# Kernel tuning notes

Hardware: AMD Instinct MI355X
Metric: run time of the kernel (lower is better)

The kernel has to match this reference:

```python
import jax, jax.numpy as jnp
import numpy as np

DATA_DIM = 768
HIDDEN = 768
STEPS = 100
DEPTH = 4          # eqx MLP depth=4 -> 4 hidden layers (3 width->width linears)
STATE = 4 * DATA_DIM
RTOL, ATOL = 1e-3, 1e-6
SAFETY, FMIN, FMAX, DT0 = 0.9, 0.2, 10.0, 0.1
INNER = 6          # bounded adaptive attempts per save interval (differentiable)

# Tsit5 Butcher tableau
A21 = 0.161
A31, A32 = -0.008480655492356989, 0.335480655492357
A41, A42, A43 = 2.8971530571054935, -6.359448489975075, 4.3622954328695815
A51, A52, A53, A54 = 5.325864828439257, -11.748883564062828, 7.4955393428898365, -0.09249506636175525
A61, A62, A63, A64, A65 = 5.86145544294642, -12.92096931784711, 8.159367898576159, -0.071584973281401, -0.028269050394068383
B1, B2, B3, B4, B5, B6 = 0.09646076681806523, 0.01, 0.4798896504144996, 1.379008574103742, -3.290069515436081, 2.324710524099774
E1, E2, E3, E4, E5, E6, E7 = -0.001780011052226, -0.000816434459657, 0.007880878010262, -0.144711007173263, 0.582357165452555, -0.458082105929187, 0.015151515151515152


def _mlp(y, W_in, b_in, W_hid, b_hid, W_out, b_out):
    h = jax.nn.softplus(W_in @ y + b_in)
    for i in range(W_hid.shape[0]):
        h = jax.nn.softplus(W_hid[i] @ h + b_hid[i])
    return W_out @ h + b_out


def _tsit5_step(f, y, dt):
    k1 = f(y)
    k2 = f(y + dt * (A21 * k1))
    k3 = f(y + dt * (A31 * k1 + A32 * k2))
    k4 = f(y + dt * (A41 * k1 + A42 * k2 + A43 * k3))
    k5 = f(y + dt * (A51 * k1 + A52 * k2 + A53 * k3 + A54 * k4))
    k6 = f(y + dt * (A61 * k1 + A62 * k2 + A63 * k3 + A64 * k4 + A65 * k5))
    y1 = y + dt * (B1 * k1 + B2 * k2 + B3 * k3 + B4 * k4 + B5 * k5 + B6 * k6)
    k7 = f(y1)
    e = dt * (E1 * k1 + E2 * k2 + E3 * k3 + E4 * k4 + E5 * k5 + E6 * k6 + E7 * k7)
    scale = ATOL + RTOL * jnp.maximum(jnp.abs(y), jnp.abs(y1))
    err = jnp.sqrt(jnp.mean((e / scale) ** 2))
    return y1, err


def _integrate(f, y0, ts):
    # adaptive Tsit5 with I-controller; step exactly to each save time
    def interval(carry, t1):
        def attempt(c, _):
            t, y, dt = c
            done = t >= t1 - 1e-10
            dt_eff = jnp.where(done, dt, jnp.minimum(dt, t1 - t))
            y1, err = _tsit5_step(f, y, dt_eff)
            accept = (err <= 1.0) & (~done)
            t_n = jnp.where(accept, t + dt_eff, t)
            y_n = jnp.where(accept, y1, y)
            factor = jnp.clip(SAFETY * jnp.maximum(err, 1e-10) ** (-0.2), FMIN, FMAX)
            dt_n = jnp.where(done, dt, dt_eff * factor)
            return (t_n, y_n, dt_n), None
        (t, y, dt), _ = jax.lax.scan(attempt, carry, None, length=INNER)
        return (t1, y, dt), y
    carry0 = (ts[0], y0, jnp.asarray(DT0, y0.dtype))
    _, ys = jax.lax.scan(interval, carry0, ts[1:])
    return jnp.concatenate([y0[None], ys], axis=0)  # [steps, STATE]


def setup_inputs() -> dict:
    key = jax.random.key(0)
    ks = jax.random.split(key, 12)

    def lin(kw, kb, fan_in, fan_out):  # equinox Linear init: U(-1/sqrt(in), 1/sqrt(in))
        lim = 1.0 / float(np.sqrt(fan_in))
        W = jax.random.uniform(kw, (fan_out, fan_in), minval=-lim, maxval=lim, dtype=jnp.float32)
        b = jax.random.uniform(kb, (fan_out,), minval=-lim, maxval=lim, dtype=jnp.float32)
        return W, b

    W_in, b_in = lin(ks[0], ks[1], STATE, HIDDEN)
    Wh, bh = [], []
    for i in range(DEPTH - 1):
        W, b = lin(ks[2 + 2 * i], ks[3 + 2 * i], HIDDEN, HIDDEN)
        Wh.append(W)
        bh.append(b)
    W_hid, b_hid = jnp.stack(Wh), jnp.stack(bh)
    W_out, b_out = lin(ks[8], ks[9], HIDDEN, STATE)
    y0 = jax.random.normal(ks[10], (STATE,), dtype=jnp.float32) * 0.01
    eps = jax.random.normal(ks[11], (STEPS, DATA_DIM), dtype=jnp.float32)
    return {"y0": y0, "W_in": W_in, "b_in": b_in, "W_hid": W_hid, "b_hid": b_hid,
            "W_out": W_out, "b_out": b_out, "eps": eps, "steps": STEPS}


def reference(y0, W_in, b_in, W_hid, b_hid, W_out, b_out, eps, steps):
    ts = jnp.linspace(0.0, 1.0, steps)
    f = lambda y: _mlp(y, W_in, b_in, W_hid, b_hid, W_out, b_out)
    ys = _integrate(f, y0, ts)                 # [steps, 4*data_dim]
    means = ys[:, :DATA_DIM]
    stddevs = ys[:, DATA_DIM:2 * DATA_DIM]
    return means + eps * stddevs               # [steps, data_dim]
```

## Files before the change

### kernel.cpp

```cpp
#include <hip/hip_runtime.h>
#include <math.h>

#define NBLK 96
#define BLK  512
#define NSTATE 3072
#define HID  768
typedef unsigned long long u64;
typedef unsigned int u32;

__device__ const float d_AT[7][6] = {
  {0.f,0.f,0.f,0.f,0.f,0.f},
  {0.161f,0.f,0.f,0.f,0.f,0.f},
  {-0.008480655492356989f,0.335480655492357f,0.f,0.f,0.f,0.f},
  {2.8971530571054935f,-6.359448489975075f,4.3622954328695815f,0.f,0.f,0.f},
  {5.325864828439257f,-11.748883564062828f,7.4955393428898365f,-0.09249506636175525f,0.f,0.f},
  {5.86145544294642f,-12.92096931784711f,8.159367898576159f,-0.071584973281401f,-0.028269050394068383f,0.f},
  {0.09646076681806523f,0.01f,0.4798896504144996f,1.379008574103742f,-3.290069515436081f,2.324710524099774f},
};
__device__ const float d_EC[7] = {
  -0.001780011052226f,-0.000816434459657f,0.007880878010262f,-0.144711007173263f,
   0.582357165452555f,-0.458082105929187f,0.015151515151515152f };

namespace {
constexpr float SBc = 0.09646076681806523f+0.01f+0.4798896504144996f
                    +1.379008574103742f+(-3.290069515436081f)+2.324710524099774f;
constexpr float SEc = -0.001780011052226f-0.000816434459657f+0.007880878010262f
                      -0.144711007173263f+0.582357165452555f-0.458082105929187f
                      +0.015151515151515152f;
}

struct GT { u64 h[2][HID]; u64 p[2][NBLK]; };
__device__ GT gt;
__device__ int g_abort;
__device__ __align__(16) float g_M[HID*HID];
__device__ float g_c0[HID];

__global__ void reset_kernel(){
  u64* w = reinterpret_cast<u64*>(&gt);
  const int n = (int)(sizeof(GT)/8);
  for (int i = blockIdx.x*blockDim.x + threadIdx.x; i < n; i += gridDim.x*blockDim.x)
    __hip_atomic_store(w + i, 0ull, __ATOMIC_RELAXED, __HIP_MEMORY_SCOPE_AGENT);
  if (blockIdx.x == 0 && threadIdx.x == 0)
    __hip_atomic_store(&g_abort, 0, __ATOMIC_RELAXED, __HIP_MEMORY_SCOPE_AGENT);
}

__global__ __launch_bounds__(512)
void prep_kernel(const float* __restrict__ Win, const float* __restrict__ Wout,
                 const float* __restrict__ bout){
  const int blk = blockIdx.x;
  const int t = threadIdx.x;
  const int rl = t >> 6, lane = t & 63;
  const int r = blk*8 + rl;
  {
    const float4* wr = reinterpret_cast<const float4*>(Win + (size_t)r*NSTATE) + lane;
    const float4* bo = reinterpret_cast<const float4*>(bout) + lane;
    float acc = 0.f;
    #pragma unroll
    for (int i = 0; i < 12; ++i){
      float4 w = wr[64*i], b = bo[64*i];
      acc = fmaf(w.x,b.x, fmaf(w.y,b.y, fmaf(w.z,b.z, fmaf(w.w,b.w, acc))));
    }
    acc += __shfl_xor(acc,32); acc += __shfl_xor(acc,16); acc += __shfl_xor(acc,8);
    acc += __shfl_xor(acc,4);  acc += __shfl_xor(acc,2);  acc += __shfl_xor(acc,1);
    if (lane == 0) g_c0[r] = acc;
  }
  const int cb = (t & 63) * 12;
  float acc[12];
  #pragma unroll
  for (int m = 0; m < 12; ++m) acc[m] = 0.f;
  const float* wrow = Win + (size_t)r*NSTATE;
  for (int i = 0; i < NSTATE; ++i){
    const float wv = wrow[i];
    const float4* wo = reinterpret_cast<const float4*>(Wout + (size_t)i*HID + cb);
    float4 a0 = wo[0], a1 = wo[1], a2 = wo[2];
    acc[0]=fmaf(wv,a0.x,acc[0]); acc[1]=fmaf(wv,a0.y,acc[1]);
    acc[2]=fmaf(wv,a0.z,acc[2]); acc[3]=fmaf(wv,a0.w,acc[3]);
    acc[4]=fmaf(wv,a1.x,acc[4]); acc[5]=fmaf(wv,a1.y,acc[5]);
    acc[6]=fmaf(wv,a1.z,acc[6]); acc[7]=fmaf(wv,a1.w,acc[7]);
    acc[8]=fmaf(wv,a2.x,acc[8]); acc[9]=fmaf(wv,a2.y,acc[9]);
    acc[10]=fmaf(wv,a2.z,acc[10]); acc[11]=fmaf(wv,a2.w,acc[11]);
  }
  #pragma unroll
  for (int m = 0; m < 12; ++m) g_M[(size_t)r*HID + cb + m] = acc[m];
}

__device__ __forceinline__ int abort_now(){
  return __hip_atomic_load(&g_abort, __ATOMIC_RELAXED, __HIP_MEMORY_SCOPE_AGENT);
}
__device__ __forceinline__ void raise_abort(){
  __hip_atomic_store(&g_abort, 1, __ATOMIC_RELAXED, __HIP_MEMORY_SCOPE_AGENT);
}
__device__ __forceinline__ void stT(u64* p, u32 tag, float v){
  u32 b; __builtin_memcpy(&b, &v, 4);
  __hip_atomic_store(p, ((u64)tag << 32) | (u64)b, __ATOMIC_RELAXED, __HIP_MEMORY_SCOPE_AGENT);
}
__device__ __forceinline__ float pollT1(const u64* p, u32 tag){
  u64* q = const_cast<u64*>(p);
  u64 w = __hip_atomic_load(q, __ATOMIC_RELAXED, __HIP_MEMORY_SCOPE_AGENT);
  u32 guard = 0;
  while ((u32)(w >> 32) != tag){
    if ((guard & 63u) == 63u && abort_now()) break;
    if (++guard > (1u<<16)){ raise_abort(); break; }
    __builtin_amdgcn_s_sleep(1);
    w = __hip_atomic_load(q, __ATOMIC_RELAXED, __HIP_MEMORY_SCOPE_AGENT);
  }
  u32 b = (u32)w; float v; __builtin_memcpy(&v, &b, 4); return v;
}
template<int NW, int CNT>
__device__ __forceinline__ void pollW(const u64* src, u32 tag, float* dst){
  const int tid = threadIdx.x;
  u64* s = const_cast<u64*>(src);
  u64 w[NW];
  #pragma unroll
  for (int r = 0; r < NW; ++r){
    const int i = tid + BLK*r;
    w[r] = (i < CNT) ? __hip_atomic_load(s + i, __ATOMIC_RELAXED, __HIP_MEMORY_SCOPE_AGENT)
                     : ((u64)tag << 32);
  }
  u32 guard = 0;
  for (;;){
    bool all = true;
    #pragma unroll
    for (int r = 0; r < NW; ++r) if ((u32)(w[r] >> 32) != tag) all = false;
    if (all) break;
    if ((guard & 63u) == 63u && abort_now()) break;
    if (++guard > (1u<<16)){ raise_abort(); break; }
    __builtin_amdgcn_s_sleep(1);
    #pragma unroll
    for (int r = 0; r < NW; ++r){
      const int i = tid + BLK*r;
      if (i < CNT && (u32)(w[r] >> 32) != tag)
        w[r] = __hip_atomic_load(s + i, __ATOMIC_RELAXED, __HIP_MEMORY_SCOPE_AGENT);
    }
  }
  #pragma unroll
  for (int r = 0; r < NW; ++r){
    const int i = tid + BLK*r;
    if (i < CNT){ u32 b = (u32)w[r]; float v; __builtin_memcpy(&v, &b, 4); dst[i] = v; }
  }
}

__device__ __forceinline__ float softplus_f(float x){
  return fmaxf(x, 0.0f) + log1pf(expf(-fabsf(x)));
}

__global__ __launch_bounds__(BLK)
void ode_kernel(const float* __restrict__ y0p,
                const float* __restrict__ Win,  const float* __restrict__ bin,
                const float* __restrict__ Whid, const float* __restrict__ bhid,
                const float* __restrict__ Wout, const float* __restrict__ bout,
                const float* __restrict__ eps,  float* __restrict__ out)
{
  __shared__ float h4s[8][HID];
  __shared__ float hsh[HID];
  __shared__ float hBs[HID], hEs[HID];
  __shared__ float us[8][8];
  __shared__ float vsl[8], b1s[8];
  __shared__ float ysl[32], y1sl[32], esl[32];
  __shared__ float red[8];
  __shared__ int s_ab;

  const int tid  = threadIdx.x, blk = blockIdx.x;
  const int wave = tid >> 6, lane = tid & 63;
  const int l16  = lane & 15;
  const int ro   = tid >> 4;
  const int row1 = blk*8 + wave;
  const int orow = (ro >> 3)*HID + blk*8 + (ro & 7);
  const int gi   = (tid >> 3)*HID + blk*8 + (tid & 7);

  float4 wr0[3], wr1[3], wr2[3], mreg[3];
  {
    const float4* b0 = reinterpret_cast<const float4*>(Whid + ((size_t)0*HID + row1)*HID) + lane;
    const float4* b1 = reinterpret_cast<const float4*>(Whid + ((size_t)1*HID + row1)*HID) + lane;
    const float4* b2 = reinterpret_cast<const float4*>(Whid + ((size_t)2*HID + row1)*HID) + lane;
    const float4* mb = reinterpret_cast<const float4*>(g_M  + (size_t)row1*HID) + lane;
    #pragma unroll
    for (int i = 0; i < 3; ++i){
      wr0[i] = b0[64*i]; wr1[i] = b1[64*i]; wr2[i] = b2[64*i]; mreg[i] = mb[64*i];
    }
  }
  const float4* wo  = reinterpret_cast<const float4*>(Wout + (size_t)orow*HID) + l16;
  const float bh0 = bhid[row1], bh1 = bhid[HID+row1], bh2 = bhid[2*HID+row1];
  const float c0r = g_c0[row1];
  const float bo_r = bout[orow];

  if (tid < 32) ysl[tid] = y0p[gi];
  if (lane == 0) b1s[wave] = bin[row1];
  if (tid < 8){ const int e = blk*8 + tid; out[e] = y0p[e] + eps[e]*y0p[HID+e]; }
  {
    float* scratch = &h4s[0][0];
    float4* d4 = reinterpret_cast<float4*>(scratch);
    const float4* s4 = reinterpret_cast<const float4*>(y0p);
    #pragma unroll
    for (int r = 0; r < 2; ++r){ const int i = tid + BLK*r; if (i < NSTATE/4) d4[i] = s4[i]; }
    __syncthreads();
    const float4* wr = reinterpret_cast<const float4*>(Win + (size_t)row1*NSTATE) + lane;
    const float4* zl = reinterpret_cast<const float4*>(scratch) + lane;
    float acc = 0.f;
    #pragma unroll
    for (int i = 0; i < 12; ++i){
      float4 w = wr[64*i], x = zl[64*i];
      acc = fmaf(w.x,x.x, fmaf(w.y,x.y, fmaf(w.z,x.z, fmaf(w.w,x.w, acc))));
    }
    acc += __shfl_xor(acc,32); acc += __shfl_xor(acc,16); acc += __shfl_xor(acc,8);
    acc += __shfl_xor(acc,4);  acc += __shfl_xor(acc,2);  acc += __shfl_xor(acc,1);
    if (lane == 0) vsl[wave] = acc;
    __syncthreads();
  }

  u32 hseq = 0, pseq = 0;
  int kpar = 0;
  auto slot = [&](int j){ return (j==1) ? (kpar?7:1) : (j==7) ? (kpar?1:7) : j; };

  auto stage = [&](int s, float dte){
    __syncthreads();
    const int tg = slot(s + 1);
    ++hseq;
    if (tid < 8){
      float a = 0.f;
      for (int j = 1; j <= s; ++j) a += d_AT[s][j-1] * us[slot(j)][tid];
      stT(&gt.h[hseq&1][blk*8 + tid], hseq, softplus_f(vsl[tid] + dte*a + b1s[tid]));
    }
    pollW<2, HID>(gt.h[hseq&1], hseq, hsh);
    __syncthreads();
    #pragma unroll
    for (int l = 0; l < 3; ++l){
      const float4* hx = reinterpret_cast<const float4*>(hsh) + lane;
      float acc = 0.f;
      #pragma unroll
      for (int i = 0; i < 3; ++i){
        float4 w = (l==0) ? wr0[i] : (l==1) ? wr1[i] : wr2[i];
        float4 x = hx[64*i];
        acc = fmaf(w.x,x.x, fmaf(w.y,x.y, fmaf(w.z,x.z, fmaf(w.w,x.w, acc))));
      }
      acc += __shfl_xor(acc,32); acc += __shfl_xor(acc,16); acc += __shfl_xor(acc,8);
      acc += __shfl_xor(acc,4);  acc += __shfl_xor(acc,2);  acc += __shfl_xor(acc,1);
      const float bh = (l==0) ? bh0 : (l==1) ? bh1 : bh2;
      ++hseq;
      if (lane == 0) stT(&gt.h[hseq&1][row1], hseq, softplus_f(acc + bh));
      __syncthreads();
      pollW<2, HID>(gt.h[hseq&1], hseq, (l < 2) ? hsh : h4s[tg]);
      __syncthreads();
    }
    {
      const float4* hx = reinterpret_cast<const float4*>(h4s[tg]) + lane;
      float acc = 0.f;
      #pragma unroll
      for (int i = 0; i < 3; ++i){
        float4 w = mreg[i], x = hx[64*i];
        acc = fmaf(w.x,x.x, fmaf(w.y,x.y, fmaf(w.z,x.z, fmaf(w.w,x.w, acc))));
      }
      acc += __shfl_xor(acc,32); acc += __shfl_xor(acc,16); acc += __shfl_xor(acc,8);
      acc += __shfl_xor(acc,4);  acc += __shfl_xor(acc,2);  acc += __shfl_xor(acc,1);
      if (lane == 0) us[tg][wave] = acc + c0r;
    }
  };

  stage(0, 0.f);

  float t = 0.f, dtv = 0.1f;
  for (int iv = 1; iv < 100; ++iv){
    const float t1 = (float)iv / 99.0f;
    for (int a = 0; a < 6; ++a){
      if (t >= t1 - 1e-10f) break;
      if (tid == 0) s_ab = abort_now();
      __syncthreads();
      if (s_ab) return;
      const float dte = fminf(dtv, t1 - t);

      stage(1,dte); stage(2,dte); stage(3,dte);
      stage(4,dte); stage(5,dte); stage(6,dte);
      __syncthreads();

      for (int c = tid; c < HID; c += BLK){
        float hb = 0.f, he = 0.f;
        for (int j = 1; j <= 6; ++j) hb = fmaf(d_AT[6][j-1], h4s[slot(j)][c], hb);
        for (int j = 1; j <= 7; ++j) he = fmaf(d_EC[j-1],    h4s[slot(j)][c], he);
        hBs[c] = hb; hEs[c] = he;
      }
      __syncthreads();
      {
        const float4* hb4 = reinterpret_cast<const float4*>(hBs) + l16;
        const float4* he4 = reinterpret_cast<const float4*>(hEs) + l16;
        float ab = 0.f, ae = 0.f;
        #pragma unroll
        for (int i = 0; i < 12; ++i){
          float4 w = wo[16*i], xb = hb4[16*i], xe = he4[16*i];
          ab = fmaf(w.x,xb.x, fmaf(w.y,xb.y, fmaf(w.z,xb.z, fmaf(w.w,xb.w, ab))));
          ae = fmaf(w.x,xe.x, fmaf(w.y,xe.y, fmaf(w.z,xe.z, fmaf(w.w,xe.w, ae))));
        }
        ab += __shfl_xor(ab,8); ab += __shfl_xor(ab,4); ab += __shfl_xor(ab,2); ab += __shfl_xor(ab,1);
        ae += __shfl_xor(ae,8); ae += __shfl_xor(ae,4); ae += __shfl_xor(ae,2); ae += __shfl_xor(ae,1);
        if (l16 == 0){
          y1sl[ro] = ysl[ro] + dte*(ab + SBc*bo_r);
          esl[ro]  = dte*(ae + SEc*bo_r);
        }
      }
      __syncthreads();
      ++pseq;
      if (tid < 32){
        const float sc = 1e-6f + 1e-3f * fmaxf(fabsf(ysl[tid]), fabsf(y1sl[tid]));
        const float q = esl[tid] / sc;
        float v = q*q;
        v += __shfl_xor(v,16); v += __shfl_xor(v,8);
        v += __shfl_xor(v,4);  v += __shfl_xor(v,2); v += __shfl_xor(v,1);
        if (tid == 0) stT(&gt.p[pseq&1][blk], pseq, v);
      }
      float v = 0.f;
      if (tid < NBLK) v = pollT1(&gt.p[pseq&1][tid], pseq);
      v += __shfl_xor(v,32); v += __shfl_xor(v,16); v += __shfl_xor(v,8);
      v += __shfl_xor(v,4);  v += __shfl_xor(v,2);  v += __shfl_xor(v,1);
      if (lane == 0) red[wave] = v;
      __syncthreads();
      const float err = sqrtf((red[0]+red[1]) * (1.0f/3072.0f));
      __syncthreads();

      const bool accept = (err <= 1.0f);
      const float factor = fminf(fmaxf(0.9f * powf(fmaxf(err, 1e-10f), -0.2f), 0.2f), 10.0f);
      if (accept){
        t += dte;
        if (tid < 32) ysl[tid] = y1sl[tid];
        if (tid < 8){
          float s = 0.f;
          for (int j = 1; j <= 6; ++j) s += d_AT[6][j-1] * us[slot(j)][tid];
          vsl[tid] += dte * s;
        }
        kpar ^= 1;
      }
      dtv = dte * factor;
      __syncthreads();
    }
    t = t1;
    if (tid < 8){
      const int m = blk*8 + tid;
      out[(size_t)iv*HID + m] = ysl[tid] + eps[(size_t)iv*HID + m] * ysl[8 + tid];
    }
    __syncthreads();
  }
}

extern "C" void kernel_launch(void* const* d_in, const int* in_sizes, int n_in,
                              void* d_out, int out_size, void* d_ws, size_t ws_size,
                              hipStream_t stream) {
  const float* y0   = (const float*)d_in[0];
  const float* Win  = (const float*)d_in[1];
  const float* bin  = (const float*)d_in[2];
  const float* Whid = (const float*)d_in[3];
  const float* bhid = (const float*)d_in[4];
  const float* Wout = (const float*)d_in[5];
  const float* bout = (const float*)d_in[6];
  const float* eps  = (const float*)d_in[7];
  float* out = (float*)d_out;
  (void)in_sizes; (void)n_in; (void)out_size; (void)d_ws; (void)ws_size;

  reset_kernel<<<dim3(4), dim3(BLK), 0, stream>>>();
  prep_kernel<<<dim3(96), dim3(512), 0, stream>>>(Win, Wout, bout);
  ode_kernel<<<dim3(NBLK), dim3(BLK), 0, stream>>>(y0, Win, bin, Whid, bhid, Wout, bout, eps, out);
}
```

Baseline: 7.839 ms.

## Halve persistent grid to 48 blocks and retile precompute GEMM with LDS-staged Win

```diff
diff --git a/kernel.cpp b/kernel.cpp
--- a/kernel.cpp
+++ b/kernel.cpp
@@ -1,7 +1,7 @@
 #include <hip/hip_runtime.h>
 #include <math.h>
 
-#define NBLK 96
+#define NBLK 48
 #define BLK  512
 #define NSTATE 3072
 #define HID  768
@@ -44,44 +44,68 @@
     __hip_atomic_store(&g_abort, 0, __ATOMIC_RELAXED, __HIP_MEMORY_SCOPE_AGENT);
 }
 
-__global__ __launch_bounds__(512)
+__global__ __launch_bounds__(512, 1)
 void prep_kernel(const float* __restrict__ Win, const float* __restrict__ Wout,
                  const float* __restrict__ bout){
+  extern __shared__ float wl[];
   const int blk = blockIdx.x;
   const int t = threadIdx.x;
-  const int rl = t >> 6, lane = t & 63;
-  const int r = blk*8 + rl;
   {
+    const float4* wsrc = reinterpret_cast<const float4*>(Win + (size_t)blk*8*NSTATE);
+    float4* wdst = reinterpret_cast<float4*>(wl);
+    for (int i = t; i < 8*NSTATE/4; i += 512) wdst[i] = wsrc[i];
+  }
+  __syncthreads();
+  const int seg = t >> 6;
+  const int cb  = (t & 63) * 12;
+  float acc[8][12];
+  #pragma unroll
+  for (int r = 0; r < 8; ++r)
+    #pragma unroll
+    for (int j = 0; j < 12; ++j) acc[r][j] = 0.f;
+  const int k0 = seg * 384;
+  for (int k = 0; k < 384; ++k){
+    const float4* wo4 = reinterpret_cast<const float4*>(Wout + (size_t)(k0 + k)*HID + cb);
+    const float4 a0 = wo4[0], a1 = wo4[1], a2 = wo4[2];
+    #pragma unroll
+    for (int r = 0; r < 8; ++r){
+      const float wv = wl[r*NSTATE + k0 + k];
+      acc[r][0]=fmaf(wv,a0.x,acc[r][0]); acc[r][1]=fmaf(wv,a0.y,acc[r][1]);
+      acc[r][2]=fmaf(wv,a0.z,acc[r][2]); acc[r][3]=fmaf(wv,a0.w,acc[r][3]);
+      acc[r][4]=fmaf(wv,a1.x,acc[r][4]); acc[r][5]=fmaf(wv,a1.y,acc[r][5]);
+      acc[r][6]=fmaf(wv,a1.z,acc[r][6]); acc[r][7]=fmaf(wv,a1.w,acc[r][7]);
+      acc[r][8]=fmaf(wv,a2.x,acc[r][8]); acc[r][9]=fmaf(wv,a2.y,acc[r][9]);
+      acc[r][10]=fmaf(wv,a2.z,acc[r][10]); acc[r][11]=fmaf(wv,a2.w,acc[r][11]);
+    }
+  }
+  __syncthreads();
+  for (int r = 0; r < 8; ++r){
+    #pragma unroll
+    for (int j = 0; j < 12; ++j) wl[seg*HID + cb + j] = acc[r][j];
+    __syncthreads();
+    for (int c = t; c < HID; c += 512){
+      float s2 = 0.f;
+      #pragma unroll
+      for (int s3 = 0; s3 < 8; ++s3) s2 += wl[s3*HID + c];
+      g_M[(size_t)(blk*8 + r)*HID + c] = s2;
+    }
+    __syncthreads();
+  }
+  {
+    const int rl = t >> 6, lane = t & 63;
+    const int r = blk*8 + rl;
     const float4* wr = reinterpret_cast<const float4*>(Win + (size_t)r*NSTATE) + lane;
     const float4* bo = reinterpret_cast<const float4*>(bout) + lane;
-    float acc = 0.f;
+    float a2c = 0.f;
     #pragma unroll
     for (int i = 0; i < 12; ++i){
       float4 w = wr[64*i], b = bo[64*i];
-      acc = fmaf(w.x,b.x, fmaf(w.y,b.y, fmaf(w.z,b.z, fmaf(w.w,b.w, acc))));
-    }
-    acc += __shfl_xor(acc,32); acc += __shfl_xor(acc,16); acc += __shfl_xor(acc,8);
-    acc += __shfl_xor(acc,4);  acc += __shfl_xor(acc,2);  acc += __shfl_xor(acc,1);
-    if (lane == 0) g_c0[r] = acc;
-  }
-  const int cb = (t & 63) * 12;
-  float acc[12];
-  #pragma unroll
-  for (int m = 0; m < 12; ++m) acc[m] = 0.f;
-  const float* wrow = Win + (size_t)r*NSTATE;
-  for (int i = 0; i < NSTATE; ++i){
-    const float wv = wrow[i];
-    const float4* wo = reinterpret_cast<const float4*>(Wout + (size_t)i*HID + cb);
-    float4 a0 = wo[0], a1 = wo[1], a2 = wo[2];
-    acc[0]=fmaf(wv,a0.x,acc[0]); acc[1]=fmaf(wv,a0.y,acc[1]);
-    acc[2]=fmaf(wv,a0.z,acc[2]); acc[3]=fmaf(wv,a0.w,acc[3]);
-    acc[4]=fmaf(wv,a1.x,acc[4]); acc[5]=fmaf(wv,a1.y,acc[5]);
-    acc[6]=fmaf(wv,a1.z,acc[6]); acc[7]=fmaf(wv,a1.w,acc[7]);
-    acc[8]=fmaf(wv,a2.x,acc[8]); acc[9]=fmaf(wv,a2.y,acc[9]);
-    acc[10]=fmaf(wv,a2.z,acc[10]); acc[11]=fmaf(wv,a2.w,acc[11]);
-  }
-  #pragma unroll
-  for (int m = 0; m < 12; ++m) g_M[(size_t)r*HID + cb + m] = acc[m];
+      a2c = fmaf(w.x,b.x, fmaf(w.y,b.y, fmaf(w.z,b.z, fmaf(w.w,b.w, a2c))));
+    }
+    a2c += __shfl_xor(a2c,32); a2c += __shfl_xor(a2c,16); a2c += __shfl_xor(a2c,8);
+    a2c += __shfl_xor(a2c,4);  a2c += __shfl_xor(a2c,2);  a2c += __shfl_xor(a2c,1);
+    if (lane == 0) g_c0[r] = a2c;
+  }
 }
 
 __device__ __forceinline__ int abort_now(){
@@ -152,41 +176,41 @@
                 const float* __restrict__ eps,  float* __restrict__ out)
 {
   __shared__ float h4s[8][HID];
-  __shared__ float hsh[HID];
+  __shared__ float hshA[HID], hshB[HID];
   __shared__ float hBs[HID], hEs[HID];
-  __shared__ float us[8][8];
-  __shared__ float vsl[8], b1s[8];
-  __shared__ float ysl[32], y1sl[32], esl[32];
-  __shared__ float red[8];
+  __shared__ float us[8][16];
+  __shared__ float vsl[16], b1s[16];
+  __shared__ float ysl[64], y1sl[64], esl[64];
+  __shared__ float red0;
   __shared__ int s_ab;
 
   const int tid  = threadIdx.x, blk = blockIdx.x;
   const int wave = tid >> 6, lane = tid & 63;
-  const int l16  = lane & 15;
-  const int ro   = tid >> 4;
-  const int row1 = blk*8 + wave;
-  const int orow = (ro >> 3)*HID + blk*8 + (ro & 7);
-  const int gi   = (tid >> 3)*HID + blk*8 + (tid & 7);
-
-  float4 wr0[3], wr1[3], wr2[3], mreg[3];
+  const int hl = lane >> 5, lane32 = lane & 31;
+  const int hrow = blk*16 + wave*2 + hl;
+  const int ro = tid >> 3, l8 = tid & 7;
+  const int orow = (ro >> 4)*HID + blk*16 + (ro & 15);
+  const int gi   = (tid >> 4)*HID + blk*16 + (tid & 15);
+
+  float4 wr0[6], wr1[6], wr2[6], mreg[6];
   {
-    const float4* b0 = reinterpret_cast<const float4*>(Whid + ((size_t)0*HID + row1)*HID) + lane;
-    const float4* b1 = reinterpret_cast<const float4*>(Whid + ((size_t)1*HID + row1)*HID) + lane;
-    const float4* b2 = reinterpret_cast<const float4*>(Whid + ((size_t)2*HID + row1)*HID) + lane;
-    const float4* mb = reinterpret_cast<const float4*>(g_M  + (size_t)row1*HID) + lane;
-    #pragma unroll
-    for (int i = 0; i < 3; ++i){
-      wr0[i] = b0[64*i]; wr1[i] = b1[64*i]; wr2[i] = b2[64*i]; mreg[i] = mb[64*i];
-    }
-  }
-  const float4* wo  = reinterpret_cast<const float4*>(Wout + (size_t)orow*HID) + l16;
-  const float bh0 = bhid[row1], bh1 = bhid[HID+row1], bh2 = bhid[2*HID+row1];
-  const float c0r = g_c0[row1];
+    const float4* b0 = reinterpret_cast<const float4*>(Whid + ((size_t)0*HID + hrow)*HID) + lane32;
+    const float4* b1 = reinterpret_cast<const float4*>(Whid + ((size_t)1*HID + hrow)*HID) + lane32;
+    const float4* b2 = reinterpret_cast<const float4*>(Whid + ((size_t)2*HID + hrow)*HID) + lane32;
+    const float4* mb = reinterpret_cast<const float4*>(g_M  + (size_t)hrow*HID) + lane32;
+    #pragma unroll
+    for (int i = 0; i < 6; ++i){
+      wr0[i] = b0[32*i]; wr1[i] = b1[32*i]; wr2[i] = b2[32*i]; mreg[i] = mb[32*i];
+    }
+  }
+  const float4* wo4 = reinterpret_cast<const float4*>(Wout + (size_t)orow*HID) + l8;
+  const float bh0 = bhid[hrow], bh1v = bhid[HID+hrow], bh2v = bhid[2*HID+hrow];
+  const float c0r = g_c0[hrow];
   const float bo_r = bout[orow];
 
-  if (tid < 32) ysl[tid] = y0p[gi];
-  if (lane == 0) b1s[wave] = bin[row1];
-  if (tid < 8){ const int e = blk*8 + tid; out[e] = y0p[e] + eps[e]*y0p[HID+e]; }
+  if (tid < 64) ysl[tid] = y0p[gi];
+  if (tid < 16) b1s[tid] = bin[blk*16 + tid];
+  if (tid < 16){ const int e = blk*16 + tid; out[e] = y0p[e] + eps[e]*y0p[HID+e]; }
   {
     float* scratch = &h4s[0][0];
     float4* d4 = reinterpret_cast<float4*>(scratch);
@@ -194,17 +218,19 @@
     #pragma unroll
     for (int r = 0; r < 2; ++r){ const int i = tid + BLK*r; if (i < NSTATE/4) d4[i] = s4[i]; }
     __syncthreads();
-    const float4* wr = reinterpret_cast<const float4*>(Win + (size_t)row1*NSTATE) + lane;
-    const float4* zl = reinterpret_cast<const float4*>(scratch) + lane;
+    const int vrow = blk*16 + (tid >> 5);
+    const int v32 = tid & 31;
+    const float4* wr = reinterpret_cast<const float4*>(Win + (size_t)vrow*NSTATE) + v32;
+    const float4* zl = reinterpret_cast<const float4*>(scratch) + v32;
     float acc = 0.f;
     #pragma unroll
-    for (int i = 0; i < 12; ++i){
-      float4 w = wr[64*i], x = zl[64*i];
+    for (int i = 0; i < 24; ++i){
+      float4 w = wr[32*i], x = zl[32*i];
       acc = fmaf(w.x,x.x, fmaf(w.y,x.y, fmaf(w.z,x.z, fmaf(w.w,x.w, acc))));
     }
-    acc += __shfl_xor(acc,32); acc += __shfl_xor(acc,16); acc += __shfl_xor(acc,8);
+    acc += __shfl_xor(acc,16); acc += __shfl_xor(acc,8);
     acc += __shfl_xor(acc,4);  acc += __shfl_xor(acc,2);  acc += __shfl_xor(acc,1);
-    if (lane == 0) vsl[wave] = acc;
+    if (v32 == 0) vsl[tid >> 5] = acc;
     __syncthreads();
   }
 
@@ -216,43 +242,43 @@
     __syncthreads();
     const int tg = slot(s + 1);
     ++hseq;
-    if (tid < 8){
+    if (tid < 16){
       float a = 0.f;
       for (int j = 1; j <= s; ++j) a += d_AT[s][j-1] * us[slot(j)][tid];
-      stT(&gt.h[hseq&1][blk*8 + tid], hseq, softplus_f(vsl[tid] + dte*a + b1s[tid]));
-    }
-    pollW<2, HID>(gt.h[hseq&1], hseq, hsh);
+      stT(&gt.h[hseq&1][blk*16 + tid], hseq, softplus_f(vsl[tid] + dte*a + b1s[tid]));
+    }
+    pollW<2, HID>(gt.h[hseq&1], hseq, hshA);
     __syncthreads();
     #pragma unroll
     for (int l = 0; l < 3; ++l){
-      const float4* hx = reinterpret_cast<const float4*>(hsh) + lane;
+      const float* rbuf = (l == 1) ? hshB : hshA;
+      const float4* hx = reinterpret_cast<const float4*>(rbuf) + lane32;
       float acc = 0.f;
       #pragma unroll
-      for (int i = 0; i < 3; ++i){
+      for (int i = 0; i < 6; ++i){
         float4 w = (l==0) ? wr0[i] : (l==1) ? wr1[i] : wr2[i];
-        float4 x = hx[64*i];
+        float4 x = hx[32*i];
         acc = fmaf(w.x,x.x, fmaf(w.y,x.y, fmaf(w.z,x.z, fmaf(w.w,x.w, acc))));
       }
-      acc += __shfl_xor(acc,32); acc += __shfl_xor(acc,16); acc += __shfl_xor(acc,8);
+      acc += __shfl_xor(acc,16); acc += __shfl_xor(acc,8);
       acc += __shfl_xor(acc,4);  acc += __shfl_xor(acc,2);  acc += __shfl_xor(acc,1);
-      const float bh = (l==0) ? bh0 : (l==1) ? bh1 : bh2;
+      const float bh = (l==0) ? bh0 : (l==1) ? bh1v : bh2v;
       ++hseq;
-      if (lane == 0) stT(&gt.h[hseq&1][row1], hseq, softplus_f(acc + bh));
-      __syncthreads();
-      pollW<2, HID>(gt.h[hseq&1], hseq, (l < 2) ? hsh : h4s[tg]);
+      if (lane32 == 0) stT(&gt.h[hseq&1][hrow], hseq, softplus_f(acc + bh));
+      pollW<2, HID>(gt.h[hseq&1], hseq, (l==0) ? hshB : (l==1) ? hshA : h4s[tg]);
       __syncthreads();
     }
     {
-      const float4* hx = reinterpret_cast<const float4*>(h4s[tg]) + lane;
+      const float4* hx = reinterpret_cast<const float4*>(h4s[tg]) + lane32;
       float acc = 0.f;
       #pragma unroll
-      for (int i = 0; i < 3; ++i){
-        float4 w = mreg[i], x = hx[64*i];
+      for (int i = 0; i < 6; ++i){
+        float4 w = mreg[i], x = hx[32*i];
         acc = fmaf(w.x,x.x, fmaf(w.y,x.y, fmaf(w.z,x.z, fmaf(w.w,x.w, acc))));
       }
-      acc += __shfl_xor(acc,32); acc += __shfl_xor(acc,16); acc += __shfl_xor(acc,8);
+      acc += __shfl_xor(acc,16); acc += __shfl_xor(acc,8);
       acc += __shfl_xor(acc,4);  acc += __shfl_xor(acc,2);  acc += __shfl_xor(acc,1);
-      if (lane == 0) us[tg][wave] = acc + c0r;
+      if (lane32 == 0) us[tg][wave*2 + hl] = acc + c0r;
     }
   };
 
@@ -280,47 +306,51 @@
       }
       __syncthreads();
       {
-        const float4* hb4 = reinterpret_cast<const float4*>(hBs) + l16;
-        const float4* he4 = reinterpret_cast<const float4*>(hEs) + l16;
+        const float4* hb4 = reinterpret_cast<const float4*>(hBs) + l8;
+        const float4* he4 = reinterpret_cast<const float4*>(hEs) + l8;
         float ab = 0.f, ae = 0.f;
         #pragma unroll
-        for (int i = 0; i < 12; ++i){
-          float4 w = wo[16*i], xb = hb4[16*i], xe = he4[16*i];
+        for (int i = 0; i < 24; ++i){
+          float4 w = wo4[8*i], xb = hb4[8*i], xe = he4[8*i];
           ab = fmaf(w.x,xb.x, fmaf(w.y,xb.y, fmaf(w.z,xb.z, fmaf(w.w,xb.w, ab))));
           ae = fmaf(w.x,xe.x, fmaf(w.y,xe.y, fmaf(w.z,xe.z, fmaf(w.w,xe.w, ae))));
         }
-        ab += __shfl_xor(ab,8); ab += __shfl_xor(ab,4); ab += __shfl_xor(ab,2); ab += __shfl_xor(ab,1);
-        ae += __shfl_xor(ae,8); ae += __shfl_xor(ae,4); ae += __shfl_xor(ae,2); ae += __shfl_xor(ae,1);
-        if (l16 == 0){
+        ab += __shfl_xor(ab,4); ab += __shfl_xor(ab,2); ab += __shfl_xor(ab,1);
+        ae += __shfl_xor(ae,4); ae += __shfl_xor(ae,2); ae += __shfl_xor(ae,1);
+        if (l8 == 0){
           y1sl[ro] = ysl[ro] + dte*(ab + SBc*bo_r);
           esl[ro]  = dte*(ae + SEc*bo_r);
         }
       }
       __syncthreads();
       ++pseq;
-      if (tid < 32){
+      if (tid < 64){
         const float sc = 1e-6f + 1e-3f * fmaxf(fabsf(ysl[tid]), fabsf(y1sl[tid]));
         const float q = esl[tid] / sc;
         float v = q*q;
-        v += __shfl_xor(v,16); v += __shfl_xor(v,8);
-        v += __shfl_xor(v,4);  v += __shfl_xor(v,2); v += __shfl_xor(v,1);
+        v += __shfl_xor(v,32); v += __shfl_xor(v,16); v += __shfl_xor(v,8);
+        v += __shfl_xor(v,4);  v += __shfl_xor(v,2);  v += __shfl_xor(v,1);
         if (tid == 0) stT(&gt.p[pseq&1][blk], pseq, v);
       }
-      float v = 0.f;
-      if (tid < NBLK) v = pollT1(&gt.p[pseq&1][tid], pseq);
-      v += __shfl_xor(v,32); v += __shfl_xor(v,16); v += __shfl_xor(v,8);
-      v += __shfl_xor(v,4);  v += __shfl_xor(v,2);  v += __shfl_xor(v,1);
-      if (lane == 0) red[wave] = v;
-      __syncthreads();
-      const float err = sqrtf((red[0]+red[1]) * (1.0f/3072.0f));
+      {
+        float v = 0.f;
+        if (tid < NBLK) v = pollT1(&gt.p[pseq&1][tid], pseq);
+        if (wave == 0){
+          v += __shfl_xor(v,32); v += __shfl_xor(v,16); v += __shfl_xor(v,8);
+          v += __shfl_xor(v,4);  v += __shfl_xor(v,2);  v += __shfl_xor(v,1);
+          if (tid == 0) red0 = v;
+        }
+      }
+      __syncthreads();
+      const float err = sqrtf(red0 * (1.0f/3072.0f));
       __syncthreads();
 
       const bool accept = (err <= 1.0f);
       const float factor = fminf(fmaxf(0.9f * powf(fmaxf(err, 1e-10f), -0.2f), 0.2f), 10.0f);
       if (accept){
         t += dte;
-        if (tid < 32) ysl[tid] = y1sl[tid];
-        if (tid < 8){
+        if (tid < 64) ysl[tid] = y1sl[tid];
+        if (tid < 16){
           float s = 0.f;
           for (int j = 1; j <= 6; ++j) s += d_AT[6][j-1] * us[slot(j)][tid];
           vsl[tid] += dte * s;
@@ -331,9 +361,9 @@
       __syncthreads();
     }
     t = t1;
-    if (tid < 8){
-      const int m = blk*8 + tid;
-      out[(size_t)iv*HID + m] = ysl[tid] + eps[(size_t)iv*HID + m] * ysl[8 + tid];
+    if (tid < 16){
+      const int m = blk*16 + tid;
+      out[(size_t)iv*HID + m] = ysl[tid] + eps[(size_t)iv*HID + m] * ysl[16 + tid];
     }
     __syncthreads();
   }
@@ -353,7 +383,10 @@
   float* out = (float*)d_out;
   (void)in_sizes; (void)n_in; (void)out_size; (void)d_ws; (void)ws_size;
 
+  const int prep_lds = 8 * NSTATE * 4;
+  (void)hipFuncSetAttribute(reinterpret_cast<const void*>(&prep_kernel),
+                            hipFuncAttributeMaxDynamicSharedMemorySize, prep_lds);
   reset_kernel<<<dim3(4), dim3(BLK), 0, stream>>>();
-  prep_kernel<<<dim3(96), dim3(512), 0, stream>>>(Win, Wout, bout);
+  prep_kernel<<<dim3(96), dim3(512), prep_lds, stream>>>(Win, Wout, bout);
   ode_kernel<<<dim3(NBLK), dim3(BLK), 0, stream>>>(y0, Win, bin, Whid, bhid, Wout, bout, eps, out);
 }
```

After: 6.932 ms. 1.13x faster.
